# Performance work log

Hardware: AMD Instinct MI355X
Metric: run time of the kernel (lower is better)

Reference implementation:

```python
import jax, jax.numpy as jnp
import numpy as np

B, N, D_IN = 8, 2048, 512
H = 1024          # MLP hidden
D_EMB = 512       # embed output dim
D_ATTN = 256      # attn_layers[-1]; KQ MLP outputs 2*D_ATTN


def setup_inputs() -> dict:
    key = jax.random.key(0)
    ks = jax.random.split(key, 9)
    s = lambda fi, fo: (2.0 / (fi + fo)) ** 0.5
    return {
        "x": jax.random.normal(ks[0], (B, N, D_IN), dtype=jnp.float32),
        # embed MLP: Linear(D_IN,H), ReLU, Linear(H,D_EMB)  (weights stored [in,out])
        "We1": jax.random.normal(ks[1], (D_IN, H), dtype=jnp.float32) * s(D_IN, H),
        "be1": jnp.zeros((H,), dtype=jnp.float32),
        "We2": jax.random.normal(ks[2], (H, D_EMB), dtype=jnp.float32) * s(H, D_EMB),
        "be2": jnp.zeros((D_EMB,), dtype=jnp.float32),
        # KQ MLP: Linear(D_IN,H), ReLU, Linear(H, 2*D_ATTN)
        "Wk1": jax.random.normal(ks[3], (D_IN, H), dtype=jnp.float32) * s(D_IN, H),
        "bk1": jnp.zeros((H,), dtype=jnp.float32),
        "Wk2": jax.random.normal(ks[4], (H, 2 * D_ATTN), dtype=jnp.float32) * s(H, 2 * D_ATTN),
        "bk2": jnp.zeros((2 * D_ATTN,), dtype=jnp.float32),
    }


def reference(x, We1, be1, We2, be2, Wk1, bk1, Wk2, bk2):
    # embed MLP
    embs = jax.nn.relu(x @ We1 + be1) @ We2 + be2            # [B,N,D_EMB]
    # KQ MLP; chunk: first half K, second half Q
    kq = jax.nn.relu(x @ Wk1 + bk1) @ Wk2 + bk2              # [B,N,2*D_ATTN]
    K, Q = kq[..., :D_ATTN], kq[..., D_ATTN:]
    # unscaled attention: softmax(Q K^T) V
    scores = jnp.einsum("bqd,bkd->bqk", Q, K)                # [B,N,N]
    A = jax.nn.softmax(scores, axis=-1)
    return jnp.einsum("bqk,bkd->bqd", A, embs)               # [B,N,D_EMB]
```

## Files before the change

### kernel.cpp

```cpp
#include <hip/hip_runtime.h>
#include <stdint.h>

using fx4   = __attribute__((ext_vector_type(4))) float;
using half8 = __attribute__((ext_vector_type(8))) _Float16;

__device__ __forceinline__ ushort f2h(float x) {
  _Float16 h = (_Float16)x;
  union { _Float16 hv; ushort u; } v; v.hv = h;
  return v.u;
}

__device__ __forceinline__ void gload_lds16(const ushort* g, ushort* l) {
  __builtin_amdgcn_global_load_lds(
      (__attribute__((address_space(1))) const void*)g,
      (__attribute__((address_space(3))) void*)l, 16, 0, 0);
}

#define MFMA16(a, b, c) __builtin_amdgcn_mfma_f32_16x16x32_f16(a, b, c, 0, 0, 0)

__device__ __forceinline__ void gemm_body(
    const ushort* __restrict__ A, int lda,
    const ushort* __restrict__ B, int ldb,
    const float* __restrict__ bias,
    void* __restrict__ C, int ldc,
    int K, int flags, int bx, int by,
    ushort* As, ushort* Bs, ushort* __restrict__ C2 = nullptr)
{
  const int tid  = threadIdx.x;
  const int lane = tid & 63;
  const int wave = tid >> 6;
  const int wm   = (wave >> 1) * 64;
  const int wn   = (wave & 1) * 64;
  const long long bm = (long long)by * 128;
  const long long bn = (long long)bx * 128;

  const int srow = tid >> 2;
  const int skq  = (tid & 3) * 8;
  const ushort* a0 = A + (bm + srow) * lda + skq;
  const ushort* a1 = a0 + 64LL * lda;
  const ushort* b0 = B + (bn + srow) * ldb + skq;
  const ushort* b1 = b0 + 64LL * ldb;
  ushort* lA0 = &As[tid * 8];
  ushort* lA1 = &As[2048 + tid * 8];
  ushort* lB0 = &Bs[tid * 8];
  ushort* lB1 = &Bs[2048 + tid * 8];

  fx4 acc[4][4] = {};
  const ushort* ap = &As[(wm + (lane & 15)) * 32 + (lane >> 4) * 8];
  const ushort* bp = &Bs[(wn + (lane & 15)) * 32 + (lane >> 4) * 8];

  for (int k0 = 0; k0 < K; k0 += 32) {
    gload_lds16(a0, lA0);
    gload_lds16(a1, lA1);
    gload_lds16(b0, lB0);
    gload_lds16(b1, lB1);
    a0 += 32; a1 += 32; b0 += 32; b1 += 32;
    __syncthreads();
    half8 af[4], bv[4];
#pragma unroll
    for (int t = 0; t < 4; ++t) {
      af[t] = *(const half8*)(ap + t * 16 * 32);
      bv[t] = *(const half8*)(bp + t * 16 * 32);
    }
#pragma unroll
    for (int i = 0; i < 4; ++i)
#pragma unroll
      for (int j = 0; j < 4; ++j)
        acc[i][j] = MFMA16(af[i], bv[j], acc[i][j]);
    __syncthreads();
  }

  const int col0 = (int)bn + wn + (lane & 15);
  const int row0 = (int)bm + wm + ((lane >> 4) << 2);

  if (flags & 16) {
    ushort* Ch = (ushort*)C;
#pragma unroll
    for (int j = 0; j < 4; ++j) {
      const int col = col0 + j * 16;
      const float bvv = bias ? bias[col] : 0.0f;
#pragma unroll
      for (int i = 0; i < 4; ++i) {
        const int row = row0 + i * 16;
        ushort4 o;
        o.x = f2h(acc[i][j][0] + bvv);
        o.y = f2h(acc[i][j][1] + bvv);
        o.z = f2h(acc[i][j][2] + bvv);
        o.w = f2h(acc[i][j][3] + bvv);
        *(ushort4*)(Ch + (long long)(row >> 5) * 16384 + (long long)col * 32 + (row & 31)) = o;
      }
    }
    return;
  }

  if (flags & 32) {
    ushort* KTp = (ushort*)C;
#pragma unroll
    for (int j = 0; j < 4; ++j) {
      const int col = col0 + j * 16;
      const float bvv = bias ? bias[col] : 0.0f;
#pragma unroll
      for (int i = 0; i < 4; ++i) {
        const int row = row0 + i * 16;
#pragma unroll
        for (int r = 0; r < 4; ++r) {
          const float v = acc[i][j][r] + bvv;
          if (col < 256) {
            const int tok = row + r;
            KTp[(long long)(tok >> 5) * 8192 + (col >> 5) * 1024 +
                (tok & 31) * 32 + (col & 31)] = f2h(v);
          } else {
            C2[(long long)(row + r) * 256 + (col - 256)] = f2h(v);
          }
        }
      }
    }
    return;
  }

  float*  Cf = (float*)C;
  ushort* Ch = (ushort*)C;
#pragma unroll
  for (int j = 0; j < 4; ++j) {
    const int col = col0 + j * 16;
    const float bvv = bias ? bias[col] : 0.0f;
#pragma unroll
    for (int i = 0; i < 4; ++i) {
      const long long row = row0 + i * 16;
#pragma unroll
      for (int r = 0; r < 4; ++r) {
        float v = acc[i][j][r] + bvv;
        if (flags & 1) v = fmaxf(v, 0.0f);
        if (flags & 2) Ch[(row + r) * ldc + col] = f2h(v);
        else           Cf[(row + r) * ldc + col] = v;
      }
    }
  }
}

__global__ __launch_bounds__(256)
void gemm_bt(const ushort* __restrict__ A, int lda, long long sA,
             const ushort* __restrict__ B, int ldb, long long sB,
             const float* __restrict__ bias,
             void* __restrict__ C, int ldc, long long sC,
             int K, int flags)
{
  __shared__ ushort As[128 * 32];
  __shared__ ushort Bs[128 * 32];
  const int z = blockIdx.z;
  void* Cz = (flags & 2) ? (void*)((ushort*)C + (long long)z * sC)
                         : (void*)((float*)C + (long long)z * sC);
  gemm_body(A + (long long)z * sA, lda, B + (long long)z * sB, ldb, bias,
            Cz, ldc, K, flags, blockIdx.x, blockIdx.y, As, Bs);
}

__global__ __launch_bounds__(256)
void gemm2_pair(const ushort* __restrict__ H, const ushort* __restrict__ W2c,
                const float* __restrict__ be2, const float* __restrict__ bk2,
                ushort* __restrict__ VT, ushort* __restrict__ KT,
                ushort* __restrict__ Qm)
{
  __shared__ ushort As[128 * 32];
  __shared__ ushort Bs[128 * 32];
  if (blockIdx.z == 0)
    gemm_body(H, 2048, W2c, 1024, be2, VT, 0, 1024, 16,
              blockIdx.x, blockIdx.y, As, Bs);
  else
    gemm_body(H + 1024, 2048, W2c + 524288, 1024, bk2, KT, 0, 1024, 32,
              blockIdx.x, blockIdx.y, As, Bs, Qm);
}

__global__ __launch_bounds__(512, 2)
void attn_fused(const ushort* __restrict__ KT, const ushort* __restrict__ VT,
                const ushort* __restrict__ Qm, float* __restrict__ out)
{
  __shared__ ushort Qs[20480];
  __shared__ ushort Ps[10240];
  __shared__ float  rmax[256];
  __shared__ float  mstate[64];
  __shared__ float  mnewA[64];
  __shared__ float  alphaA[64];
  __shared__ float  lred[256];

  const int tid  = threadIdx.x;
  const int lane = tid & 63;
  const int w    = tid >> 6;
  const int c    = lane & 15;
  const int q4   = lane >> 4;
  const int qw   = w >> 2;
  const int tw   = w & 3;
  const int dw   = w * 64;
  const int z    = blockIdx.x;
  const long long tb = (long long)z * 2048;
  const long long pbase = (long long)z * 64;
  const int q0   = blockIdx.y * 64;

#pragma unroll
  for (int p = 0; p < 4; ++p) {
    const int cu  = p * 512 + tid;
    const int row = cu >> 5;
    const int kch = cu & 31;
    const int dc  = kch >> 2, qg = kch & 3;
    const half8 v = *(const half8*)(Qm + (tb + q0 + row) * 256 + dc * 32 + qg * 8);
    *(half8*)(Qs + dc * 2560 + row * 40 + qg * 8) = v;
  }
  if (tid < 64) mstate[tid] = -3.0e38f;
  __syncthreads();

  float l_part[2][4] = {};
  fx4 o[4][4] = {};

  for (int t0 = 0; t0 < 2048; t0 += 128) {
    const long long pt = pbase + (t0 >> 5);
    half8 kb[2][8];
    const ushort* kp = KT + (pt + tw) * 8192;
#pragma unroll
    for (int dc = 0; dc < 8; ++dc) {
      kb[0][dc] = *(const half8*)(kp + dc * 1024 + c * 32 + q4 * 8);
      kb[1][dc] = *(const half8*)(kp + dc * 1024 + (16 + c) * 32 + q4 * 8);
    }
    fx4 s[2][2] = {};
#pragma unroll
    for (int dc = 0; dc < 8; ++dc) {
      const half8 a0 = *(const half8*)(Qs + dc * 2560 + (qw * 32 + c) * 40 + q4 * 8);
      const half8 a1 = *(const half8*)(Qs + dc * 2560 + (qw * 32 + 16 + c) * 40 + q4 * 8);
      s[0][0] = MFMA16(a0, kb[0][dc], s[0][0]); s[0][1] = MFMA16(a0, kb[1][dc], s[0][1]);
      s[1][0] = MFMA16(a1, kb[0][dc], s[1][0]); s[1][1] = MFMA16(a1, kb[1][dc], s[1][1]);
    }
    half8 vb[4][4];
#pragma unroll
    for (int kc = 0; kc < 4; ++kc)
#pragma unroll
      for (int n = 0; n < 4; ++n)
        vb[kc][n] = *(const half8*)(VT + (pt + kc) * 16384 +
                                    (dw + n * 16 + c) * 32 + q4 * 8);
#pragma unroll
    for (int i = 0; i < 2; ++i) {
      fx4 rm;
#pragma unroll
      for (int r = 0; r < 4; ++r) rm[r] = fmaxf(s[i][0][r], s[i][1][r]);
#pragma unroll
      for (int off = 1; off < 16; off <<= 1)
#pragma unroll
        for (int r = 0; r < 4; ++r) rm[r] = fmaxf(rm[r], __shfl_xor(rm[r], off, 64));
      if (c == 0) {
#pragma unroll
        for (int r = 0; r < 4; ++r)
          rmax[tw * 64 + qw * 32 + i * 16 + q4 * 4 + r] = rm[r];
      }
    }
    __syncthreads();
    if (w == 0) {
      const float mo = mstate[lane];
      float mn = fmaxf(fmaxf(rmax[lane], rmax[64 + lane]),
                       fmaxf(rmax[128 + lane], rmax[192 + lane]));
      mn = fmaxf(mn, mo);
      mnewA[lane]  = mn;
      alphaA[lane] = __expf(mo - mn);
      mstate[lane] = mn;
    }
    __syncthreads();
#pragma unroll
    for (int i = 0; i < 2; ++i)
#pragma unroll
      for (int r = 0; r < 4; ++r) {
        const int q = qw * 32 + i * 16 + q4 * 4 + r;
        const float mn = mnewA[q];
        const float e0 = __expf(s[i][0][r] - mn);
        const float e1 = __expf(s[i][1][r] - mn);
        l_part[i][r] = alphaA[q] * l_part[i][r] + e0 + e1;
        Ps[tw * 2560 + q * 40 + c]      = f2h(e0);
        Ps[tw * 2560 + q * 40 + 16 + c] = f2h(e1);
      }
#pragma unroll
    for (int i4 = 0; i4 < 4; ++i4)
#pragma unroll
      for (int r = 0; r < 4; ++r) {
        const float aq = alphaA[i4 * 16 + q4 * 4 + r];
#pragma unroll
        for (int n = 0; n < 4; ++n) o[i4][n][r] *= aq;
      }
    __syncthreads();
#pragma unroll
    for (int kc = 0; kc < 4; ++kc) {
      half8 pa[4];
#pragma unroll
      for (int i4 = 0; i4 < 4; ++i4)
        pa[i4] = *(const half8*)(Ps + kc * 2560 + (i4 * 16 + c) * 40 + q4 * 8);
#pragma unroll
      for (int i4 = 0; i4 < 4; ++i4)
#pragma unroll
        for (int n = 0; n < 4; ++n)
          o[i4][n] = MFMA16(pa[i4], vb[kc][n], o[i4][n]);
    }
  }

#pragma unroll
  for (int i = 0; i < 2; ++i) {
    fx4 lv;
#pragma unroll
    for (int r = 0; r < 4; ++r) lv[r] = l_part[i][r];
#pragma unroll
    for (int off = 1; off < 16; off <<= 1)
#pragma unroll
      for (int r = 0; r < 4; ++r) lv[r] += __shfl_xor(lv[r], off, 64);
    if (c == 0) {
#pragma unroll
      for (int r = 0; r < 4; ++r)
        lred[tw * 64 + qw * 32 + i * 16 + q4 * 4 + r] = lv[r];
    }
  }
  __syncthreads();
  if (w == 0)
    alphaA[lane] = 1.0f / (lred[lane] + lred[64 + lane] + lred[128 + lane] + lred[192 + lane]);
  __syncthreads();

  float* ob = out + (tb + q0) * 512 + dw;
#pragma unroll
  for (int i4 = 0; i4 < 4; ++i4)
#pragma unroll
    for (int r = 0; r < 4; ++r) {
      const int q = i4 * 16 + q4 * 4 + r;
      const float li = alphaA[q];
#pragma unroll
      for (int n = 0; n < 4; ++n)
        ob[(long long)q * 512 + n * 16 + c] = o[i4][n][r] * li;
    }
}

__global__ __launch_bounds__(256)
void transpose_cast_w2(const float* __restrict__ in0, const float* __restrict__ in1,
                       ushort* __restrict__ out0, ushort* __restrict__ out1,
                       int R, int C) {
  __shared__ float tile[32][33];
  const float* in  = blockIdx.z ? in1 : in0;
  ushort*      outp = blockIdx.z ? out1 : out0;
  const int c0 = blockIdx.x * 32, r0 = blockIdx.y * 32;
  const int tx = threadIdx.x & 31, ty = threadIdx.x >> 5;
#pragma unroll
  for (int i = 0; i < 32; i += 8)
    tile[ty + i][tx] = in[(long long)(r0 + ty + i) * C + (c0 + tx)];
  __syncthreads();
#pragma unroll
  for (int i = 0; i < 32; i += 8)
    outp[(long long)(c0 + ty + i) * R + (r0 + tx)] = f2h(tile[tx][ty + i]);
}

__global__ __launch_bounds__(256)
void cast_f32_f16(const float* __restrict__ in, ushort* __restrict__ out) {
  const long long i = ((long long)blockIdx.x * 256 + threadIdx.x) * 4;
  const float4 v = *(const float4*)(in + i);
  ushort4 o;
  o.x = f2h(v.x); o.y = f2h(v.y); o.z = f2h(v.z); o.w = f2h(v.w);
  *(ushort4*)(out + i) = o;
}

__global__ __launch_bounds__(256)
void concat_bias(const float* __restrict__ b0, const float* __restrict__ b1,
                 float* __restrict__ out) {
  const int i = blockIdx.x * 256 + threadIdx.x;
  out[i] = (i < 1024) ? b0[i] : b1[i - 1024];
}

extern "C" void kernel_launch(void* const* d_in, const int* in_sizes, int n_in,
                              void* d_out, int out_size, void* d_ws, size_t ws_size,
                              hipStream_t stream) {
  (void)in_sizes; (void)n_in; (void)out_size; (void)ws_size;
  const float* x   = (const float*)d_in[0];
  const float* We1 = (const float*)d_in[1];
  const float* be1 = (const float*)d_in[2];
  const float* We2 = (const float*)d_in[3];
  const float* be2 = (const float*)d_in[4];
  const float* Wk1 = (const float*)d_in[5];
  const float* bk1 = (const float*)d_in[6];
  const float* Wk2 = (const float*)d_in[7];
  const float* bk2 = (const float*)d_in[8];
  float* out = (float*)d_out;
  char* ws = (char*)d_ws;

  ushort* Xb  = (ushort*)(ws + 0);
  ushort* W2c = (ushort*)(ws + 0);
  ushort* H   = (ushort*)(ws + 16777216);
  ushort* VT  = (ushort*)(ws + 83886080);
  ushort* KT  = (ushort*)(ws + 100663296);
  ushort* Qm  = (ushort*)(ws + 109051904);
  float*  b1c = (float*)(ws + 117440512);
  ushort* W1c = (ushort*)(ws + 117448704);

  cast_f32_f16<<<dim3(8192), 256, 0, stream>>>(x, Xb);
  transpose_cast_w2<<<dim3(32, 16, 2), 256, 0, stream>>>(We1, Wk1, W1c, W1c + 524288, 512, 1024);
  concat_bias<<<dim3(8), 256, 0, stream>>>(be1, bk1, b1c);

  gemm_bt<<<dim3(16, 128, 1), 256, 0, stream>>>(Xb, 512, 0, W1c, 512, 0, b1c,
                                                H, 2048, 0, 512, 1 | 2);

  transpose_cast_w2<<<dim3(16, 32, 2), 256, 0, stream>>>(We2, Wk2, W2c, W2c + 524288, 1024, 512);

  gemm2_pair<<<dim3(4, 128, 2), 256, 0, stream>>>(H, W2c, be2, bk2, VT, KT, Qm);

  attn_fused<<<dim3(8, 32), 512, 0, stream>>>(KT, VT, Qm, out);
}
```

Baseline: 315.0 us.

## Halve attention query tile to 32 rows to double block count

Shrinks the per-block query tile in the fused attention kernel from 64 to 32 rows. The grid doubles to 512 blocks, and launch bounds ask for 4 blocks per CU. The aim is to fill all CUs (the old 256-block grid underfills a 256-CU part) and cut per-thread register and LDS use. In exchange, each K/V tile is reloaded by twice as many blocks, raising global/L2 traffic, and each loaded K/V fragment feeds fewer MFMAs.

```diff
diff --git a/kernel.cpp b/kernel.cpp
--- a/kernel.cpp
+++ b/kernel.cpp
@@ -170,17 +170,17 @@
               blockIdx.x, blockIdx.y, As, Bs, Qm);
 }
 
-__global__ __launch_bounds__(512, 2)
+__global__ __launch_bounds__(512, 4)
 void attn_fused(const ushort* __restrict__ KT, const ushort* __restrict__ VT,
                 const ushort* __restrict__ Qm, float* __restrict__ out)
 {
-  __shared__ ushort Qs[20480];
-  __shared__ ushort Ps[10240];
-  __shared__ float  rmax[256];
-  __shared__ float  mstate[64];
-  __shared__ float  mnewA[64];
-  __shared__ float  alphaA[64];
-  __shared__ float  lred[256];
+  __shared__ ushort Qs[10240];
+  __shared__ ushort Ps[5120];
+  __shared__ float  rmax[128];
+  __shared__ float  mstate[32];
+  __shared__ float  mnewA[32];
+  __shared__ float  alphaA[32];
+  __shared__ float  lred[128];
 
   const int tid  = threadIdx.x;
   const int lane = tid & 63;
@@ -193,22 +193,22 @@
   const int z    = blockIdx.x;
   const long long tb = (long long)z * 2048;
   const long long pbase = (long long)z * 64;
-  const int q0   = blockIdx.y * 64;
-
-#pragma unroll
-  for (int p = 0; p < 4; ++p) {
+  const int q0   = blockIdx.y * 32;
+
+#pragma unroll
+  for (int p = 0; p < 2; ++p) {
     const int cu  = p * 512 + tid;
     const int row = cu >> 5;
     const int kch = cu & 31;
     const int dc  = kch >> 2, qg = kch & 3;
     const half8 v = *(const half8*)(Qm + (tb + q0 + row) * 256 + dc * 32 + qg * 8);
-    *(half8*)(Qs + dc * 2560 + row * 40 + qg * 8) = v;
-  }
-  if (tid < 64) mstate[tid] = -3.0e38f;
+    *(half8*)(Qs + dc * 1280 + row * 40 + qg * 8) = v;
+  }
+  if (tid < 32) mstate[tid] = -3.0e38f;
   __syncthreads();
 
-  float l_part[2][4] = {};
-  fx4 o[4][4] = {};
+  float l_part[4] = {};
+  fx4 o[2][4] = {};
 
   for (int t0 = 0; t0 < 2048; t0 += 128) {
     const long long pt = pbase + (t0 >> 5);
@@ -219,13 +219,12 @@
       kb[0][dc] = *(const half8*)(kp + dc * 1024 + c * 32 + q4 * 8);
       kb[1][dc] = *(const half8*)(kp + dc * 1024 + (16 + c) * 32 + q4 * 8);
     }
-    fx4 s[2][2] = {};
+    fx4 s[2] = {};
 #pragma unroll
     for (int dc = 0; dc < 8; ++dc) {
-      const half8 a0 = *(const half8*)(Qs + dc * 2560 + (qw * 32 + c) * 40 + q4 * 8);
-      const half8 a1 = *(const half8*)(Qs + dc * 2560 + (qw * 32 + 16 + c) * 40 + q4 * 8);
-      s[0][0] = MFMA16(a0, kb[0][dc], s[0][0]); s[0][1] = MFMA16(a0, kb[1][dc], s[0][1]);
-      s[1][0] = MFMA16(a1, kb[0][dc], s[1][0]); s[1][1] = MFMA16(a1, kb[1][dc], s[1][1]);
+      const half8 a0 = *(const half8*)(Qs + dc * 1280 + (qw * 16 + c) * 40 + q4 * 8);
+      s[0] = MFMA16(a0, kb[0][dc], s[0]);
+      s[1] = MFMA16(a0, kb[1][dc], s[1]);
     }
     half8 vb[4][4];
 #pragma unroll
@@ -234,11 +233,10 @@
       for (int n = 0; n < 4; ++n)
         vb[kc][n] = *(const half8*)(VT + (pt + kc) * 16384 +
                                     (dw + n * 16 + c) * 32 + q4 * 8);
-#pragma unroll
-    for (int i = 0; i < 2; ++i) {
+    {
       fx4 rm;
 #pragma unroll
-      for (int r = 0; r < 4; ++r) rm[r] = fmaxf(s[i][0][r], s[i][1][r]);
+      for (int r = 0; r < 4; ++r) rm[r] = fmaxf(s[0][r], s[1][r]);
 #pragma unroll
       for (int off = 1; off < 16; off <<= 1)
 #pragma unroll
@@ -246,34 +244,32 @@
       if (c == 0) {
 #pragma unroll
         for (int r = 0; r < 4; ++r)
-          rmax[tw * 64 + qw * 32 + i * 16 + q4 * 4 + r] = rm[r];
-      }
-    }
-    __syncthreads();
-    if (w == 0) {
-      const float mo = mstate[lane];
-      float mn = fmaxf(fmaxf(rmax[lane], rmax[64 + lane]),
-                       fmaxf(rmax[128 + lane], rmax[192 + lane]));
+          rmax[tw * 32 + qw * 16 + q4 * 4 + r] = rm[r];
+      }
+    }
+    __syncthreads();
+    if (tid < 32) {
+      const float mo = mstate[tid];
+      float mn = fmaxf(fmaxf(rmax[tid], rmax[32 + tid]),
+                       fmaxf(rmax[64 + tid], rmax[96 + tid]));
       mn = fmaxf(mn, mo);
-      mnewA[lane]  = mn;
-      alphaA[lane] = __expf(mo - mn);
-      mstate[lane] = mn;
-    }
-    __syncthreads();
-#pragma unroll
-    for (int i = 0; i < 2; ++i)
-#pragma unroll
-      for (int r = 0; r < 4; ++r) {
-        const int q = qw * 32 + i * 16 + q4 * 4 + r;
-        const float mn = mnewA[q];
-        const float e0 = __expf(s[i][0][r] - mn);
-        const float e1 = __expf(s[i][1][r] - mn);
-        l_part[i][r] = alphaA[q] * l_part[i][r] + e0 + e1;
-        Ps[tw * 2560 + q * 40 + c]      = f2h(e0);
-        Ps[tw * 2560 + q * 40 + 16 + c] = f2h(e1);
-      }
-#pragma unroll
-    for (int i4 = 0; i4 < 4; ++i4)
+      mnewA[tid]  = mn;
+      alphaA[tid] = __expf(mo - mn);
+      mstate[tid] = mn;
+    }
+    __syncthreads();
+#pragma unroll
+    for (int r = 0; r < 4; ++r) {
+      const int q = qw * 16 + q4 * 4 + r;
+      const float mn = mnewA[q];
+      const float e0 = __expf(s[0][r] - mn);
+      const float e1 = __expf(s[1][r] - mn);
+      l_part[r] = alphaA[q] * l_part[r] + e0 + e1;
+      Ps[tw * 1280 + q * 40 + c]      = f2h(e0);
+      Ps[tw * 1280 + q * 40 + 16 + c] = f2h(e1);
+    }
+#pragma unroll
+    for (int i4 = 0; i4 < 2; ++i4)
 #pragma unroll
       for (int r = 0; r < 4; ++r) {
         const float aq = alphaA[i4 * 16 + q4 * 4 + r];
@@ -283,23 +279,22 @@
     __syncthreads();
 #pragma unroll
     for (int kc = 0; kc < 4; ++kc) {
-      half8 pa[4];
-#pragma unroll
-      for (int i4 = 0; i4 < 4; ++i4)
-        pa[i4] = *(const half8*)(Ps + kc * 2560 + (i4 * 16 + c) * 40 + q4 * 8);
-#pragma unroll
-      for (int i4 = 0; i4 < 4; ++i4)
+      half8 pa[2];
+#pragma unroll
+      for (int i4 = 0; i4 < 2; ++i4)
+        pa[i4] = *(const half8*)(Ps + kc * 1280 + (i4 * 16 + c) * 40 + q4 * 8);
+#pragma unroll
+      for (int i4 = 0; i4 < 2; ++i4)
 #pragma unroll
         for (int n = 0; n < 4; ++n)
           o[i4][n] = MFMA16(pa[i4], vb[kc][n], o[i4][n]);
     }
   }
 
-#pragma unroll
-  for (int i = 0; i < 2; ++i) {
+  {
     fx4 lv;
 #pragma unroll
-    for (int r = 0; r < 4; ++r) lv[r] = l_part[i][r];
+    for (int r = 0; r < 4; ++r) lv[r] = l_part[r];
 #pragma unroll
     for (int off = 1; off < 16; off <<= 1)
 #pragma unroll
@@ -307,17 +302,17 @@
     if (c == 0) {
 #pragma unroll
       for (int r = 0; r < 4; ++r)
-        lred[tw * 64 + qw * 32 + i * 16 + q4 * 4 + r] = lv[r];
+        lred[tw * 32 + qw * 16 + q4 * 4 + r] = lv[r];
     }
   }
   __syncthreads();
-  if (w == 0)
-    alphaA[lane] = 1.0f / (lred[lane] + lred[64 + lane] + lred[128 + lane] + lred[192 + lane]);
+  if (tid < 32)
+    alphaA[tid] = 1.0f / (lred[tid] + lred[32 + tid] + lred[64 + tid] + lred[96 + tid]);
   __syncthreads();
 
   float* ob = out + (tb + q0) * 512 + dw;
 #pragma unroll
-  for (int i4 = 0; i4 < 4; ++i4)
+  for (int i4 = 0; i4 < 2; ++i4)
 #pragma unroll
     for (int r = 0; r < 4; ++r) {
       const int q = i4 * 16 + q4 * 4 + r;
@@ -398,5 +393,5 @@
 
   gemm2_pair<<<dim3(4, 128, 2), 256, 0, stream>>>(H, W2c, be2, bk2, VT, KT, Qm);
 
-  attn_fused<<<dim3(8, 32), 512, 0, stream>>>(KT, VT, Qm, out);
-}
+  attn_fused<<<dim3(8, 64), 512, 0, stream>>>(KT, VT, Qm, out);
+}
```

Result: slower. 377.1 us (+19.7%).
